# Kernel tuning notes

Measured on AMD Instinct MI355X. Metric: run time of the kernel, lower is better.

The kernel has to match this reference:

```python
import jax, jax.numpy as jnp
import numpy as np

B, N, K = 4, 4096, 16
C_IN, C_OUT = 128, 128
H1, H2 = 256, 256
IN_SZ = 2 * C_IN  # key_feats='self' -> concat(self feats, neighbor feats)


def setup_inputs() -> dict:
    key = jax.random.key(0)
    ks = jax.random.split(key, 12)
    s = 1.0 / np.sqrt(IN_SZ)
    inp = {
        "keys": jax.random.normal(ks[0], (B, N, 3), jnp.float32),
        "points": jax.random.normal(ks[1], (B, N, 3), jnp.float32),
        "feats": jax.random.normal(ks[2], (B, N, C_IN), jnp.float32),
        "n_idxs": jax.random.randint(ks[3], (B, N, K), 0, N, jnp.int32),
        "neighbor_valid": jax.random.randint(ks[4], (B, N, K), 0, 2, jnp.int32),
        "W1": jax.random.uniform(ks[5], (IN_SZ, H1), jnp.float32, -s, s),
        "b1": jnp.zeros((H1,), jnp.float32),
        "W2": jax.random.uniform(ks[6], (H1, H2), jnp.float32, -1/np.sqrt(H1), 1/np.sqrt(H1)),
        "b2": jnp.zeros((H2,), jnp.float32),
        "W3": jax.random.uniform(ks[7], (H2, C_OUT), jnp.float32, -1/np.sqrt(H2), 1/np.sqrt(H2)),
        "b3": jnp.zeros((C_OUT,), jnp.float32),
    }
    return inp


def reference(keys, points, feats, n_idxs, neighbor_valid, W1, b1, W2, b2, W3, b3):
    # gather neighbor features: feats[bb, n_idxs] -> [B, N, K, C_IN]
    bb = jnp.arange(feats.shape[0])[:, None, None]
    neighbor_feats = feats[bb, n_idxs]
    # key_feats='self': broadcast query's own feats over neighbor dim, concat
    exp_feats = jnp.broadcast_to(feats[:, :, None, :], neighbor_feats.shape)
    pairs = jnp.concatenate([exp_feats, neighbor_feats], axis=-1)  # [B,N,K,2C]
    # SetTransform MLP per edge (reduction='none')
    h = jax.nn.relu(jnp.einsum("bnki,ih->bnkh", pairs, W1) + b1)
    h = jax.nn.relu(jnp.einsum("bnkh,hj->bnkj", h, W2) + b2)
    edges = jnp.einsum("bnkj,jo->bnko", h, W3) + b3  # [B,N,K,C_OUT]
    # mask invalid neighbors and reduce over neighbor dim
    mask = neighbor_valid[..., None].astype(edges.dtype)
    reduced = jnp.sum(edges * mask, axis=2)  # [B,N,C_OUT]
    return reduced
```

## Files before the change

### kernel.cpp

```cpp
#include <hip/hip_runtime.h>
#include <hip/hip_bf16.h>
#include <stdint.h>

#define Bb 4
#define Nn 4096
#define Kk 16
#define Cc 128
#define Hh 256
#define BN 16384

typedef __attribute__((ext_vector_type(4))) float f32x4;
typedef __attribute__((ext_vector_type(8))) short s16x8;

__device__ __forceinline__ unsigned short f2bf(float f) {
  union { float f; unsigned u; } v; v.f = f;
  unsigned r = v.u + 0x7FFFu + ((v.u >> 16) & 1u);
  return (unsigned short)(r >> 16);
}
__device__ __forceinline__ float bf2f(unsigned short s) {
  union { unsigned u; float f; } v; v.u = ((unsigned)s) << 16;
  return v.f;
}
__device__ __forceinline__ s16x8 ld16(const unsigned short* p) {
  return *(const s16x8*)p;
}

#define MFMA16(a, b, c) __builtin_amdgcn_mfma_f32_16x16x32_bf16((a), (b), (c), 0, 0, 0)

__global__ void pack_kernel(const float* __restrict__ feats,
                            const float* __restrict__ W1,
                            const float* __restrict__ W2,
                            const float* __restrict__ W3,
                            unsigned short* __restrict__ featsb,
                            unsigned short* __restrict__ W1p,
                            unsigned short* __restrict__ W2p,
                            unsigned short* __restrict__ W3p) {
  int blk = blockIdx.x, t = threadIdx.x;
  if (blk < 1024) {
    int i = (blk * 256 + t) * 8;
    const float4* fp = (const float4*)(feats + i);
    float4 f0 = fp[0], f1 = fp[1];
    uint4 o;
    o.x = (unsigned)f2bf(f0.x) | ((unsigned)f2bf(f0.y) << 16);
    o.y = (unsigned)f2bf(f0.z) | ((unsigned)f2bf(f0.w) << 16);
    o.z = (unsigned)f2bf(f1.x) | ((unsigned)f2bf(f1.y) << 16);
    o.w = (unsigned)f2bf(f1.z) | ((unsigned)f2bf(f1.w) << 16);
    *(uint4*)(featsb + i) = o;
  } else if (blk < 1056) {
    int f = (blk - 1024) * 256 + t;
    int l = f & 63, ct = (f >> 6) & 31, kt = f >> 11;
    int col = ct * 16 + (l & 15);
    int k0 = kt * 32 + ((l >> 4) << 3);
    unsigned short tmp[8];
#pragma unroll
    for (int j = 0; j < 8; ++j) {
      int k = k0 + j;
      float v = (col < 256) ? W1[k * 256 + col]
                            : W1[(128 + k) * 256 + (col - 256)];
      tmp[j] = f2bf(v);
    }
    *(uint4*)(W1p + f * 8) = *(uint4*)tmp;
  } else if (blk < 1088) {
    int f = (blk - 1056) * 256 + t;
    int l = f & 63, ct = (f >> 6) & 15, kt = f >> 10;
    int col = ct * 16 + (l & 15);
    int k0 = kt * 32 + ((l >> 4) << 3);
    unsigned short tmp[8];
#pragma unroll
    for (int j = 0; j < 8; ++j) tmp[j] = f2bf(W2[(k0 + j) * 256 + col]);
    *(uint4*)(W2p + f * 8) = *(uint4*)tmp;
  } else {
    int f = (blk - 1088) * 256 + t;
    int l = f & 63, ct = (f >> 6) & 7, kt = f >> 9;
    int col = ct * 16 + (l & 15);
    int k0 = kt * 32 + ((l >> 4) << 3);
    unsigned short tmp[8];
#pragma unroll
    for (int j = 0; j < 8; ++j) tmp[j] = f2bf(W3[(k0 + j) * 128 + col]);
    *(uint4*)(W3p + f * 8) = *(uint4*)tmp;
  }
}

__global__ __launch_bounds__(256, 2) void k1_gemm(
    const unsigned short* __restrict__ featsb,
    const unsigned short* __restrict__ W1p,
    const float* __restrict__ b1,
    unsigned short* __restrict__ A_ws,
    unsigned short* __restrict__ B_ws) {
  int m0 = blockIdx.x * 64;
  int t = threadIdx.x, w = t >> 6, l = t & 63;
  int lr = l & 15, lg = l >> 4;
  f32x4 zero4 = {0.f, 0.f, 0.f, 0.f};
  f32x4 acc[4][8];
#pragma unroll
  for (int i = 0; i < 4; ++i)
#pragma unroll
    for (int j = 0; j < 8; ++j) acc[i][j] = zero4;

  for (int kt = 0; kt < 4; ++kt) {
    s16x8 a[4];
#pragma unroll
    for (int rt = 0; rt < 4; ++rt)
      a[rt] = ld16(featsb + (m0 + rt * 16 + lr) * 128 + kt * 32 + lg * 8);
#pragma unroll
    for (int ctl = 0; ctl < 8; ++ctl) {
      int ct = w * 8 + ctl;
      s16x8 bf = ld16(W1p + (((kt * 32 + ct) * 64) + l) * 8);
#pragma unroll
      for (int rt = 0; rt < 4; ++rt)
        acc[rt][ctl] = MFMA16(a[rt], bf, acc[rt][ctl]);
    }
  }
#pragma unroll
  for (int ctl = 0; ctl < 8; ++ctl) {
    int n = w * 128 + ctl * 16 + lr;
    float bias = (n < 256) ? b1[n] : 0.f;
    unsigned short* dst = (n < 256) ? (A_ws + n) : (B_ws + (n - 256));
#pragma unroll
    for (int rt = 0; rt < 4; ++rt) {
#pragma unroll
      for (int reg = 0; reg < 4; ++reg) {
        int row = m0 + rt * 16 + lg * 4 + reg;
        dst[row * 256] = f2bf(acc[rt][ctl][reg] + bias);
      }
    }
  }
}

__global__ __launch_bounds__(256, 2) void k2_fused(
    const unsigned short* __restrict__ A_ws,
    const unsigned short* __restrict__ B_ws,
    const unsigned short* __restrict__ W2p,
    const unsigned short* __restrict__ W3p,
    const int* __restrict__ n_idxs,
    const int* __restrict__ valid,
    const float* __restrict__ b2,
    const float* __restrict__ b3,
    float* __restrict__ out) {
  __shared__ unsigned short h1s[128 * 256];
  __shared__ unsigned short gs[16 * 256];
  __shared__ float validf[128];
  __shared__ float nvalidf[8];
  char* h1b = (char*)h1s;
  char* gb = (char*)gs;

  int wg = blockIdx.x, t = threadIdx.x;
  int w = t >> 6, l = t & 63, lr = l & 15, lg = l >> 4;
  int qbase = wg * 8;
  int bN = (qbase >> 12) << 12;
  int ebase = wg * 128;

  if (t < 128) validf[t] = (float)valid[ebase + t];

#pragma unroll
  for (int i = 0; i < 16; ++i) {
    int c = i * 256 + t;
    int r = c >> 5, cc = c & 31;
    int nb = n_idxs[ebase + r];
    s16x8 av = ld16(A_ws + (qbase + (r >> 4)) * 256 + cc * 8);
    s16x8 bv = ld16(B_ws + (bN + nb) * 256 + cc * 8);
    s16x8 hv;
#pragma unroll
    for (int j = 0; j < 8; ++j) {
      float v = bf2f((unsigned short)av[j]) + bf2f((unsigned short)bv[j]);
      hv[j] = (short)f2bf(fmaxf(v, 0.f));
    }
    int off = (r * 512 + cc * 16) ^ ((r & 7) << 4);
    *(s16x8*)(h1b + off) = hv;
  }
  __syncthreads();
  if (t < 8) {
    float s = 0.f;
    for (int k = 0; k < 16; ++k) s += validf[t * 16 + k];
    nvalidf[t] = s;
  }

  f32x4 zero4 = {0.f, 0.f, 0.f, 0.f};
  f32x4 acc[8][4];
#pragma unroll
  for (int i = 0; i < 8; ++i)
#pragma unroll
    for (int j = 0; j < 4; ++j) acc[i][j] = zero4;

  for (int kt = 0; kt < 8; ++kt) {
    s16x8 a[8];
#pragma unroll
    for (int rt = 0; rt < 8; ++rt) {
      int r = rt * 16 + lr;
      int off = (r * 512 + kt * 64 + lg * 16) ^ ((r & 7) << 4);
      a[rt] = *(const s16x8*)(h1b + off);
    }
#pragma unroll
    for (int ctl = 0; ctl < 4; ++ctl) {
      int ct = w * 4 + ctl;
      s16x8 bf = ld16(W2p + (((kt * 16 + ct) * 64) + l) * 8);
#pragma unroll
      for (int rt = 0; rt < 8; ++rt)
        acc[rt][ctl] = MFMA16(a[rt], bf, acc[rt][ctl]);
    }
  }

#pragma unroll
  for (int ctl = 0; ctl < 4; ++ctl) {
    int col = w * 64 + ctl * 16 + lr;
    float bias = b2[col];
#pragma unroll
    for (int rt = 0; rt < 8; ++rt) {
      float s = 0.f;
#pragma unroll
      for (int reg = 0; reg < 4; ++reg) {
        float v = fmaxf(acc[rt][ctl][reg] + bias, 0.f);
        s += v * validf[rt * 16 + lg * 4 + reg];
      }
      s += __shfl_xor(s, 16);
      s += __shfl_xor(s, 32);
      if (l < 16) {
        int off = (rt * 512 + col * 2) ^ ((rt & 7) << 4);
        *(unsigned short*)(gb + off) = f2bf(s);
      }
    }
  }
  __syncthreads();

  f32x4 acc3[2];
  acc3[0] = zero4;
  acc3[1] = zero4;
  for (int kt = 0; kt < 8; ++kt) {
    int off = (lr * 512 + kt * 64 + lg * 16) ^ ((lr & 7) << 4);
    s16x8 a = *(const s16x8*)(gb + off);
#pragma unroll
    for (int ctl = 0; ctl < 2; ++ctl) {
      int ct = w * 2 + ctl;
      s16x8 bf = ld16(W3p + (((kt * 8 + ct) * 64) + l) * 8);
      acc3[ctl] = MFMA16(a, bf, acc3[ctl]);
    }
  }
#pragma unroll
  for (int ctl = 0; ctl < 2; ++ctl) {
    int col = w * 32 + ctl * 16 + lr;
    float bias = b3[col];
#pragma unroll
    for (int reg = 0; reg < 4; ++reg) {
      int q = lg * 4 + reg;
      if (q < 8)
        out[(qbase + q) * Cc + col] = acc3[ctl][reg] + nvalidf[q] * bias;
    }
  }
}

extern "C" void kernel_launch(void* const* d_in, const int* in_sizes, int n_in,
                              void* d_out, int out_size, void* d_ws, size_t ws_size,
                              hipStream_t stream) {
  const float* feats = (const float*)d_in[2];
  const int* n_idxs = (const int*)d_in[3];
  const int* valid = (const int*)d_in[4];
  const float* W1 = (const float*)d_in[5];
  const float* b1 = (const float*)d_in[6];
  const float* W2 = (const float*)d_in[7];
  const float* b2 = (const float*)d_in[8];
  const float* W3 = (const float*)d_in[9];
  const float* b3 = (const float*)d_in[10];
  float* out = (float*)d_out;

  char* ws = (char*)d_ws;
  unsigned short* A_ws   = (unsigned short*)(ws);
  unsigned short* B_ws   = (unsigned short*)(ws + (8u << 20));
  unsigned short* featsb = (unsigned short*)(ws + (16u << 20));
  unsigned short* W1p    = (unsigned short*)(ws + (20u << 20));
  unsigned short* W2p    = (unsigned short*)(ws + (20u << 20) + (128u << 10));
  unsigned short* W3p    = (unsigned short*)(ws + (20u << 20) + (256u << 10));

  pack_kernel<<<1104, 256, 0, stream>>>(feats, W1, W2, W3, featsb, W1p, W2p, W3p);
  k1_gemm<<<256, 256, 0, stream>>>(featsb, W1p, b1, A_ws, B_ws);
  k2_fused<<<2048, 256, 0, stream>>>(A_ws, B_ws, W2p, W3p, n_idxs, valid, b2, b3, out);
}
```

Before: 155.6 us.

## Fuse feats conversion into GEMM1, zero invalid edges, and split k2 into 512-thread halves

Drops the separate bf16 conversion of feats; the first GEMM now converts fp32 feats in registers and stages its output through LDS so A/B workspace stores are coalesced. The fused edge kernel moves to 512 threads with a half-size h1 LDS buffer processed in two K passes. Invalid edges are zeroed in h1 instead of weighting after layer 2, with the bias of those rows corrected through precomputed t3/u3 vectors. Rounding uses a cheaper perm-based conversion. The aim is fewer launches, less global traffic, more occupancy and cheaper epilogues, at the cost of an extra barrier and a bias identity that relies on b1 being absent from B and ReLU(b2) for zero rows.

```diff
diff --git a/kernel.cpp b/kernel.cpp
--- a/kernel.cpp
+++ b/kernel.cpp
@@ -1,53 +1,47 @@
 #include <hip/hip_runtime.h>
-#include <hip/hip_bf16.h>
 #include <stdint.h>
 
-#define Bb 4
-#define Nn 4096
-#define Kk 16
 #define Cc 128
-#define Hh 256
-#define BN 16384
 
 typedef __attribute__((ext_vector_type(4))) float f32x4;
 typedef __attribute__((ext_vector_type(8))) short s16x8;
 
-__device__ __forceinline__ unsigned short f2bf(float f) {
-  union { float f; unsigned u; } v; v.f = f;
-  unsigned r = v.u + 0x7FFFu + ((v.u >> 16) & 1u);
+__device__ __forceinline__ unsigned int asu(float f) { union { float f; unsigned int u; } v; v.f = f; return v.u; }
+__device__ __forceinline__ float asf(unsigned int u) { union { unsigned int u; float f; } v; v.u = u; return v.f; }
+
+__device__ __forceinline__ unsigned short f2bf_rne(float f) {
+  unsigned int u = asu(f);
+  unsigned int r = u + 0x7FFFu + ((u >> 16) & 1u);
   return (unsigned short)(r >> 16);
 }
-__device__ __forceinline__ float bf2f(unsigned short s) {
-  union { unsigned u; float f; } v; v.u = ((unsigned)s) << 16;
-  return v.f;
-}
-__device__ __forceinline__ s16x8 ld16(const unsigned short* p) {
-  return *(const s16x8*)p;
+
+__device__ __forceinline__ unsigned int pk2(float lo, float hi) {
+  return __builtin_amdgcn_perm(asu(hi) + 0x8000u, asu(lo) + 0x8000u, 0x07060302u);
+}
+
+__device__ __forceinline__ unsigned int cvt1(unsigned int a, unsigned int b) {
+  float alo = asf(a << 16), ahi = asf(a & 0xFFFF0000u);
+  float blo = asf(b << 16), bhi = asf(b & 0xFFFF0000u);
+  float lo = fmaxf(alo + blo, 0.f);
+  float hi = fmaxf(ahi + bhi, 0.f);
+  return pk2(lo, hi);
 }
 
 #define MFMA16(a, b, c) __builtin_amdgcn_mfma_f32_16x16x32_bf16((a), (b), (c), 0, 0, 0)
 
-__global__ void pack_kernel(const float* __restrict__ feats,
-                            const float* __restrict__ W1,
+__global__ void pack_kernel(const float* __restrict__ W1,
                             const float* __restrict__ W2,
                             const float* __restrict__ W3,
-                            unsigned short* __restrict__ featsb,
+                            const float* __restrict__ b2,
+                            const float* __restrict__ b3,
                             unsigned short* __restrict__ W1p,
                             unsigned short* __restrict__ W2p,
-                            unsigned short* __restrict__ W3p) {
+                            unsigned short* __restrict__ W3p,
+                            float* __restrict__ t3v,
+                            float* __restrict__ u3v) {
   int blk = blockIdx.x, t = threadIdx.x;
-  if (blk < 1024) {
-    int i = (blk * 256 + t) * 8;
-    const float4* fp = (const float4*)(feats + i);
-    float4 f0 = fp[0], f1 = fp[1];
-    uint4 o;
-    o.x = (unsigned)f2bf(f0.x) | ((unsigned)f2bf(f0.y) << 16);
-    o.y = (unsigned)f2bf(f0.z) | ((unsigned)f2bf(f0.w) << 16);
-    o.z = (unsigned)f2bf(f1.x) | ((unsigned)f2bf(f1.y) << 16);
-    o.w = (unsigned)f2bf(f1.z) | ((unsigned)f2bf(f1.w) << 16);
-    *(uint4*)(featsb + i) = o;
-  } else if (blk < 1056) {
-    int f = (blk - 1024) * 256 + t;
+  if (blk < 32) {
+    int f = blk * 256 + t;
     int l = f & 63, ct = (f >> 6) & 31, kt = f >> 11;
     int col = ct * 16 + (l & 15);
     int k0 = kt * 32 + ((l >> 4) << 3);
@@ -55,41 +49,48 @@
 #pragma unroll
     for (int j = 0; j < 8; ++j) {
       int k = k0 + j;
-      float v = (col < 256) ? W1[k * 256 + col]
-                            : W1[(128 + k) * 256 + (col - 256)];
-      tmp[j] = f2bf(v);
+      float v = (col < 256) ? W1[k * 256 + col] : W1[(128 + k) * 256 + (col - 256)];
+      tmp[j] = f2bf_rne(v);
     }
     *(uint4*)(W1p + f * 8) = *(uint4*)tmp;
-  } else if (blk < 1088) {
-    int f = (blk - 1056) * 256 + t;
+  } else if (blk < 64) {
+    int f = (blk - 32) * 256 + t;
     int l = f & 63, ct = (f >> 6) & 15, kt = f >> 10;
     int col = ct * 16 + (l & 15);
     int k0 = kt * 32 + ((l >> 4) << 3);
     unsigned short tmp[8];
 #pragma unroll
-    for (int j = 0; j < 8; ++j) tmp[j] = f2bf(W2[(k0 + j) * 256 + col]);
+    for (int j = 0; j < 8; ++j) tmp[j] = f2bf_rne(W2[(k0 + j) * 256 + col]);
     *(uint4*)(W2p + f * 8) = *(uint4*)tmp;
-  } else {
-    int f = (blk - 1088) * 256 + t;
+  } else if (blk < 80) {
+    int f = (blk - 64) * 256 + t;
     int l = f & 63, ct = (f >> 6) & 7, kt = f >> 9;
     int col = ct * 16 + (l & 15);
     int k0 = kt * 32 + ((l >> 4) << 3);
     unsigned short tmp[8];
 #pragma unroll
-    for (int j = 0; j < 8; ++j) tmp[j] = f2bf(W3[(k0 + j) * 128 + col]);
+    for (int j = 0; j < 8; ++j) tmp[j] = f2bf_rne(W3[(k0 + j) * 128 + col]);
     *(uint4*)(W3p + f * 8) = *(uint4*)tmp;
+  } else {
+    if (t < 128) {
+      float s = 0.f;
+      for (int j = 0; j < 256; ++j) s += fmaxf(b2[j], 0.f) * W3[j * 128 + t];
+      t3v[t] = b3[t] + s;
+      u3v[t] = 16.f * s;
+    }
   }
 }
 
 __global__ __launch_bounds__(256, 2) void k1_gemm(
-    const unsigned short* __restrict__ featsb,
+    const float* __restrict__ feats,
     const unsigned short* __restrict__ W1p,
     const float* __restrict__ b1,
     unsigned short* __restrict__ A_ws,
     unsigned short* __restrict__ B_ws) {
+  __shared__ __attribute__((aligned(16))) unsigned short cs[64 * 512];
+  char* cb = (char*)cs;
   int m0 = blockIdx.x * 64;
-  int t = threadIdx.x, w = t >> 6, l = t & 63;
-  int lr = l & 15, lg = l >> 4;
+  int t = threadIdx.x, w = t >> 6, l = t & 63, lr = l & 15, lg = l >> 4;
   f32x4 zero4 = {0.f, 0.f, 0.f, 0.f};
   f32x4 acc[4][8];
 #pragma unroll
@@ -100,34 +101,54 @@
   for (int kt = 0; kt < 4; ++kt) {
     s16x8 a[4];
 #pragma unroll
-    for (int rt = 0; rt < 4; ++rt)
-      a[rt] = ld16(featsb + (m0 + rt * 16 + lr) * 128 + kt * 32 + lg * 8);
+    for (int rt = 0; rt < 4; ++rt) {
+      const float* fr = feats + (m0 + rt * 16 + lr) * 128 + kt * 32 + lg * 8;
+      float4 f0 = *(const float4*)fr;
+      float4 f1 = *(const float4*)(fr + 4);
+      uint4 pk;
+      pk.x = pk2(f0.x, f0.y);
+      pk.y = pk2(f0.z, f0.w);
+      pk.z = pk2(f1.x, f1.y);
+      pk.w = pk2(f1.z, f1.w);
+      *(uint4*)&a[rt] = pk;
+    }
 #pragma unroll
     for (int ctl = 0; ctl < 8; ++ctl) {
-      int ct = w * 8 + ctl;
-      s16x8 bf = ld16(W1p + (((kt * 32 + ct) * 64) + l) * 8);
+      s16x8 bf = *(const s16x8*)(W1p + (((kt * 32) + (w * 8 + ctl)) * 64 + l) * 8);
 #pragma unroll
       for (int rt = 0; rt < 4; ++rt)
         acc[rt][ctl] = MFMA16(a[rt], bf, acc[rt][ctl]);
     }
   }
+
 #pragma unroll
   for (int ctl = 0; ctl < 8; ++ctl) {
-    int n = w * 128 + ctl * 16 + lr;
-    float bias = (n < 256) ? b1[n] : 0.f;
-    unsigned short* dst = (n < 256) ? (A_ws + n) : (B_ws + (n - 256));
+    int col = w * 128 + ctl * 16 + lr;
+    float bias = (col < 256) ? b1[col] : 0.f;
 #pragma unroll
     for (int rt = 0; rt < 4; ++rt) {
 #pragma unroll
       for (int reg = 0; reg < 4; ++reg) {
-        int row = m0 + rt * 16 + lg * 4 + reg;
-        dst[row * 256] = f2bf(acc[rt][ctl][reg] + bias);
+        int node = rt * 16 + lg * 4 + reg;
+        float v = acc[rt][ctl][reg] + bias;
+        unsigned short bv = (unsigned short)((asu(v) + 0x8000u) >> 16);
+        *(unsigned short*)(cb + ((node * 1024 + col * 2) ^ ((node & 7) << 4))) = bv;
       }
     }
   }
-}
-
-__global__ __launch_bounds__(256, 2) void k2_fused(
+  __syncthreads();
+#pragma unroll
+  for (int i = 0; i < 16; ++i) {
+    int row = i * 4 + w;
+    uint4 v = *(const uint4*)(cb + row * 1024 + ((l * 16) ^ ((row & 7) << 4)));
+    int node = m0 + row;
+    unsigned short* dst = (l < 32) ? (A_ws + node * 256 + l * 8)
+                                   : (B_ws + node * 256 + (l - 32) * 8);
+    *(uint4*)dst = v;
+  }
+}
+
+__global__ __launch_bounds__(512, 4) void k2_fused(
     const unsigned short* __restrict__ A_ws,
     const unsigned short* __restrict__ B_ws,
     const unsigned short* __restrict__ W2p,
@@ -135,115 +156,116 @@
     const int* __restrict__ n_idxs,
     const int* __restrict__ valid,
     const float* __restrict__ b2,
-    const float* __restrict__ b3,
+    const float* __restrict__ t3v,
+    const float* __restrict__ u3v,
     float* __restrict__ out) {
-  __shared__ unsigned short h1s[128 * 256];
-  __shared__ unsigned short gs[16 * 256];
-  __shared__ float validf[128];
-  __shared__ float nvalidf[8];
+  __shared__ __attribute__((aligned(16))) unsigned short h1s[128 * 128];
+  __shared__ __attribute__((aligned(16))) unsigned short gs[16 * 264];
+  __shared__ float nvf[8];
   char* h1b = (char*)h1s;
   char* gb = (char*)gs;
 
-  int wg = blockIdx.x, t = threadIdx.x;
+  int t = threadIdx.x;
   int w = t >> 6, l = t & 63, lr = l & 15, lg = l >> 4;
-  int qbase = wg * 8;
-  int bN = (qbase >> 12) << 12;
-  int ebase = wg * 128;
-
-  if (t < 128) validf[t] = (float)valid[ebase + t];
-
-#pragma unroll
-  for (int i = 0; i < 16; ++i) {
-    int c = i * 256 + t;
-    int r = c >> 5, cc = c & 31;
-    int nb = n_idxs[ebase + r];
-    s16x8 av = ld16(A_ws + (qbase + (r >> 4)) * 256 + cc * 8);
-    s16x8 bv = ld16(B_ws + (bN + nb) * 256 + cc * 8);
-    s16x8 hv;
-#pragma unroll
-    for (int j = 0; j < 8; ++j) {
-      float v = bf2f((unsigned short)av[j]) + bf2f((unsigned short)bv[j]);
-      hv[j] = (short)f2bf(fmaxf(v, 0.f));
-    }
-    int off = (r * 512 + cc * 16) ^ ((r & 7) << 4);
-    *(s16x8*)(h1b + off) = hv;
-  }
-  __syncthreads();
+  int wg = blockIdx.x;
+  int qbase = wg * 8, ebase = wg * 128;
+  int bN = qbase & ~4095;
+
+  if (t < 256) {
+    int row = 8 + (t >> 5), ch = t & 31;
+    *(f32x4*)(gb + row * 528 + ch * 16) = f32x4{0.f, 0.f, 0.f, 0.f};
+  }
   if (t < 8) {
-    float s = 0.f;
-    for (int k = 0; k < 16; ++k) s += validf[t * 16 + k];
-    nvalidf[t] = s;
-  }
+    int s = 0;
+#pragma unroll
+    for (int k = 0; k < 16; ++k) s += valid[ebase + t * 16 + k];
+    nvf[t] = (float)s;
+  }
+
+  int r = t >> 2, sub = t & 3;
+  int nb = n_idxs[ebase + r];
+  bool vld = valid[ebase + r] != 0;
+  const unsigned short* pa = A_ws + (qbase + (r >> 4)) * 256 + sub * 32;
+  const unsigned short* pb = B_ws + (bN + nb) * 256 + sub * 32;
+  int wbase = r * 256 + sub * 64;
+  int swz = (r & 7) << 4;
+  int rswz = (lr & 7) << 4;
 
   f32x4 zero4 = {0.f, 0.f, 0.f, 0.f};
-  f32x4 acc[8][4];
-#pragma unroll
-  for (int i = 0; i < 8; ++i)
-#pragma unroll
-    for (int j = 0; j < 4; ++j) acc[i][j] = zero4;
-
-  for (int kt = 0; kt < 8; ++kt) {
-    s16x8 a[8];
+  f32x4 acc[8][2];
+#pragma unroll
+  for (int i = 0; i < 8; ++i) {
+    acc[i][0] = zero4;
+    acc[i][1] = zero4;
+  }
+
+  for (int p = 0; p < 2; ++p) {
+#pragma unroll
+    for (int i = 0; i < 4; ++i) {
+      uint4 av = *(const uint4*)(pa + p * 128 + i * 8);
+      uint4 bv = *(const uint4*)(pb + p * 128 + i * 8);
+      uint4 o;
+      o.x = cvt1(av.x, bv.x);
+      o.y = cvt1(av.y, bv.y);
+      o.z = cvt1(av.z, bv.z);
+      o.w = cvt1(av.w, bv.w);
+      if (!vld) { o.x = 0u; o.y = 0u; o.z = 0u; o.w = 0u; }
+      *(uint4*)(h1b + ((wbase + i * 16) ^ swz)) = o;
+    }
+    __syncthreads();
+#pragma unroll
+    for (int kt = 0; kt < 4; ++kt) {
+      s16x8 a[8];
+      int kofs = (kt * 64 + lg * 16) ^ rswz;
+#pragma unroll
+      for (int rt = 0; rt < 8; ++rt)
+        a[rt] = *(const s16x8*)(h1b + (rt * 16 + lr) * 256 + kofs);
+      int ktg = p * 4 + kt;
+#pragma unroll
+      for (int ctl = 0; ctl < 2; ++ctl) {
+        s16x8 bf = *(const s16x8*)(W2p + (((ktg * 16) + (w * 2 + ctl)) * 64 + l) * 8);
+#pragma unroll
+        for (int rt = 0; rt < 8; ++rt)
+          acc[rt][ctl] = MFMA16(a[rt], bf, acc[rt][ctl]);
+      }
+    }
+    __syncthreads();
+  }
+
+  float bias0 = b2[w * 32 + lr];
+  float bias1 = b2[w * 32 + 16 + lr];
+#pragma unroll
+  for (int ctl = 0; ctl < 2; ++ctl) {
+    int col = w * 32 + ctl * 16 + lr;
+    float bias = ctl ? bias1 : bias0;
 #pragma unroll
     for (int rt = 0; rt < 8; ++rt) {
-      int r = rt * 16 + lr;
-      int off = (r * 512 + kt * 64 + lg * 16) ^ ((r & 7) << 4);
-      a[rt] = *(const s16x8*)(h1b + off);
-    }
-#pragma unroll
-    for (int ctl = 0; ctl < 4; ++ctl) {
-      int ct = w * 4 + ctl;
-      s16x8 bf = ld16(W2p + (((kt * 16 + ct) * 64) + l) * 8);
-#pragma unroll
-      for (int rt = 0; rt < 8; ++rt)
-        acc[rt][ctl] = MFMA16(a[rt], bf, acc[rt][ctl]);
-    }
-  }
-
-#pragma unroll
-  for (int ctl = 0; ctl < 4; ++ctl) {
-    int col = w * 64 + ctl * 16 + lr;
-    float bias = b2[col];
-#pragma unroll
-    for (int rt = 0; rt < 8; ++rt) {
-      float s = 0.f;
-#pragma unroll
-      for (int reg = 0; reg < 4; ++reg) {
-        float v = fmaxf(acc[rt][ctl][reg] + bias, 0.f);
-        s += v * validf[rt * 16 + lg * 4 + reg];
-      }
+      float s = fmaxf(acc[rt][ctl][0] + bias, 0.f)
+              + fmaxf(acc[rt][ctl][1] + bias, 0.f)
+              + fmaxf(acc[rt][ctl][2] + bias, 0.f)
+              + fmaxf(acc[rt][ctl][3] + bias, 0.f);
       s += __shfl_xor(s, 16);
       s += __shfl_xor(s, 32);
-      if (l < 16) {
-        int off = (rt * 512 + col * 2) ^ ((rt & 7) << 4);
-        *(unsigned short*)(gb + off) = f2bf(s);
-      }
+      if (l < 16)
+        *(unsigned short*)(gb + rt * 528 + col * 2) = f2bf_rne(s);
     }
   }
   __syncthreads();
 
-  f32x4 acc3[2];
-  acc3[0] = zero4;
-  acc3[1] = zero4;
+  f32x4 acc3 = zero4;
+#pragma unroll
   for (int kt = 0; kt < 8; ++kt) {
-    int off = (lr * 512 + kt * 64 + lg * 16) ^ ((lr & 7) << 4);
-    s16x8 a = *(const s16x8*)(gb + off);
-#pragma unroll
-    for (int ctl = 0; ctl < 2; ++ctl) {
-      int ct = w * 2 + ctl;
-      s16x8 bf = ld16(W3p + (((kt * 8 + ct) * 64) + l) * 8);
-      acc3[ctl] = MFMA16(a, bf, acc3[ctl]);
-    }
-  }
-#pragma unroll
-  for (int ctl = 0; ctl < 2; ++ctl) {
-    int col = w * 32 + ctl * 16 + lr;
-    float bias = b3[col];
+    s16x8 a = *(const s16x8*)(gb + lr * 528 + kt * 64 + lg * 16);
+    s16x8 bf = *(const s16x8*)(W3p + ((kt * 8 + w) * 64 + l) * 8);
+    acc3 = MFMA16(a, bf, acc3);
+  }
+  int col = w * 16 + lr;
+  if (lg < 2) {
+    float tt = t3v[col], uu = u3v[col];
 #pragma unroll
     for (int reg = 0; reg < 4; ++reg) {
       int q = lg * 4 + reg;
-      if (q < 8)
-        out[(qbase + q) * Cc + col] = acc3[ctl][reg] + nvalidf[q] * bias;
+      out[(qbase + q) * Cc + col] = acc3[reg] + nvf[q] * tt - uu;
     }
   }
 }
@@ -263,14 +285,15 @@
   float* out = (float*)d_out;
 
   char* ws = (char*)d_ws;
-  unsigned short* A_ws   = (unsigned short*)(ws);
-  unsigned short* B_ws   = (unsigned short*)(ws + (8u << 20));
-  unsigned short* featsb = (unsigned short*)(ws + (16u << 20));
-  unsigned short* W1p    = (unsigned short*)(ws + (20u << 20));
-  unsigned short* W2p    = (unsigned short*)(ws + (20u << 20) + (128u << 10));
-  unsigned short* W3p    = (unsigned short*)(ws + (20u << 20) + (256u << 10));
-
-  pack_kernel<<<1104, 256, 0, stream>>>(feats, W1, W2, W3, featsb, W1p, W2p, W3p);
-  k1_gemm<<<256, 256, 0, stream>>>(featsb, W1p, b1, A_ws, B_ws);
-  k2_fused<<<2048, 256, 0, stream>>>(A_ws, B_ws, W2p, W3p, n_idxs, valid, b2, b3, out);
-}
+  unsigned short* A_ws = (unsigned short*)(ws);
+  unsigned short* B_ws = (unsigned short*)(ws + (8u << 20));
+  unsigned short* W1p  = (unsigned short*)(ws + (16u << 20));
+  unsigned short* W2p  = (unsigned short*)(ws + (16u << 20) + (128u << 10));
+  unsigned short* W3p  = (unsigned short*)(ws + (16u << 20) + (256u << 10));
+  float* t3v = (float*)(ws + (16u << 20) + (320u << 10));
+  float* u3v = (float*)(ws + (16u << 20) + (321u << 10));
+
+  pack_kernel<<<81, 256, 0, stream>>>(W1, W2, W3, b2, b3, W1p, W2p, W3p, t3v, u3v);
+  k1_gemm<<<256, 256, 0, stream>>>(feats, W1p, b1, A_ws, B_ws);
+  k2_fused<<<2048, 512, 0, stream>>>(A_ws, B_ws, W2p, W3p, n_idxs, valid, b2, t3v, u3v, out);
+}
```

Result: slower. 160.0 us (+2.9%).
